# Optimization experiments

Measured on AMD Instinct MI355X. Metric: run time of the kernel, lower is better.

The kernel has to match this reference:

```python
import jax, jax.numpy as jnp
import numpy as np

D_MODEL = 1024
N_HEADS = 16
D_HEAD = 64
D_FF = 4096
WINDOW = 256
B, T = 2, 2048


def setup_inputs() -> dict:
    key = jax.random.key(0)
    ks = jax.random.split(key, 10)
    tot = N_HEADS * D_HEAD
    def w(k, shape):
        # approximate kaiming_normal_ fan_out init: std = sqrt(2/fan_out)
        fan_out = shape[0]
        return jax.random.normal(k, shape, jnp.float32) * np.sqrt(2.0 / fan_out)
    return {
        "x": jax.random.normal(ks[0], (B, T, D_MODEL), jnp.float32),
        "ln1_w": jnp.ones((D_MODEL,), jnp.float32),
        "qkv_w": w(ks[1], (3 * tot, D_MODEL)),
        "gate_w": w(ks[2], (tot, D_MODEL)),
        "out_w": w(ks[3], (D_MODEL, tot)),
        "ln2_w": jnp.ones((D_MODEL,), jnp.float32),
        "wg": w(ks[4], (D_FF, D_MODEL)),
        "wu": w(ks[5], (D_FF, D_MODEL)),
        "wo": w(ks[6], (D_MODEL, D_FF)),
    }


def _rmsnorm(x, w):
    return x * jax.lax.rsqrt(jnp.mean(x * x, axis=-1, keepdims=True) + 1e-6) * w


def _attention(x, qkv_w, gate_w, out_w):
    Bq, Tq, _ = x.shape
    tot = N_HEADS * D_HEAD
    qkv = x @ qkv_w.T  # [B,T,3*tot]
    q, k, v = jnp.split(qkv, 3, axis=-1)
    q = q.reshape(Bq, Tq, N_HEADS, D_HEAD).transpose(0, 2, 1, 3)
    k = k.reshape(Bq, Tq, N_HEADS, D_HEAD).transpose(0, 2, 1, 3)
    v = v.reshape(Bq, Tq, N_HEADS, D_HEAD).transpose(0, 2, 1, 3)
    scale = D_HEAD ** -0.5
    scores = jnp.einsum("bhqd,bhkd->bhqk", q, k) * scale
    pos = jnp.arange(Tq)
    dist = pos[:, None] - pos[None, :]
    allowed = (dist >= 0) & (dist < WINDOW)  # causal sliding window
    mask = jnp.where(allowed, 0.0, -jnp.inf).astype(scores.dtype)
    attn = jax.nn.softmax(scores + mask[None, None], axis=-1)
    out = jnp.einsum("bhqk,bhkd->bhqd", attn, v)
    out = out.transpose(0, 2, 1, 3).reshape(Bq, Tq, tot)
    gate = jax.nn.sigmoid(x @ gate_w.T)
    return (out * gate) @ out_w.T


def reference(x, ln1_w, qkv_w, gate_w, out_w, ln2_w, wg, wu, wo):
    x = x + _attention(_rmsnorm(x, ln1_w), qkv_w, gate_w, out_w)
    h = _rmsnorm(x, ln2_w)
    ffn = (jax.nn.silu(h @ wg.T) * (h @ wu.T)) @ wo.T
    return x + ffn
```

## Files before the change

kernel.cpp:

```cpp
#include <hip/hip_runtime.h>


#define DEV __device__ __forceinline__

using u16 = unsigned short;
typedef __attribute__((ext_vector_type(8))) short  short8;
typedef __attribute__((ext_vector_type(4))) float  floatx4;

DEV u16 f2bf(float f) {
  unsigned u = __builtin_bit_cast(unsigned, f);
  u += 0x7FFFu + ((u >> 16) & 1u);
  return (u16)(u >> 16);
}
DEV float bf2f(u16 h) {
  unsigned u = ((unsigned)h) << 16;
  return __builtin_bit_cast(float, u);
}
DEV floatx4 mfma16(short8 a, short8 b, floatx4 c) {
  return __builtin_amdgcn_mfma_f32_16x16x32_bf16(a, b, c, 0, 0, 0);
}
DEV void gload16(const u16* g, u16* lds_base_wave_uniform) {
  __builtin_amdgcn_global_load_lds(
      (const __attribute__((address_space(1))) void*)g,
      (__attribute__((address_space(3))) void*)lds_base_wave_uniform,
      16, 0, 0);
}

__global__ __launch_bounds__(256) void cvt_k(const float* __restrict__ in,
                                             u16* __restrict__ o) {
  const size_t i = (size_t)blockIdx.x * 256 + threadIdx.x;
  const float4 v = ((const float4*)in)[i];
  ushort4 r;
  r.x = f2bf(v.x); r.y = f2bf(v.y); r.z = f2bf(v.z); r.w = f2bf(v.w);
  ((ushort4*)o)[i] = r;
}

__global__ __launch_bounds__(256) void rmsnorm_k(const float* __restrict__ x,
                                                 const float* __restrict__ wt,
                                                 u16* __restrict__ o) {
  __shared__ float red[4];
  const int row = blockIdx.x;
  const int tid = threadIdx.x;
  const float4 v = ((const float4*)(x + (size_t)row * 1024))[tid];
  float ss = v.x * v.x + v.y * v.y + v.z * v.z + v.w * v.w;
  ss += __shfl_xor(ss, 1, 64);
  ss += __shfl_xor(ss, 2, 64);
  ss += __shfl_xor(ss, 4, 64);
  ss += __shfl_xor(ss, 8, 64);
  ss += __shfl_xor(ss, 16, 64);
  ss += __shfl_xor(ss, 32, 64);
  if ((tid & 63) == 0) red[tid >> 6] = ss;
  __syncthreads();
  const float tot = red[0] + red[1] + red[2] + red[3];
  const float sc = rsqrtf(tot * (1.0f / 1024.0f) + 1e-6f);
  const float4 wv = ((const float4*)wt)[tid];
  ushort4 r;
  r.x = f2bf(v.x * sc * wv.x);
  r.y = f2bf(v.y * sc * wv.y);
  r.z = f2bf(v.z * sc * wv.z);
  r.w = f2bf(v.w * sc * wv.w);
  ((ushort4*)(o + (size_t)row * 1024))[tid] = r;
}

template <int EPI>
__global__ __launch_bounds__(256) void gemm_bf16_k(
    const u16* __restrict__ A, const u16* __restrict__ B, int N, int K,
    u16* __restrict__ cb, float* __restrict__ cf,
    const u16* __restrict__ aux, const float* __restrict__ resid) {
  __shared__ __align__(16) u16 As[2][4096];
  __shared__ __align__(16) u16 Bs[2][4096];

  const int tid = threadIdx.x;
  const int w = tid >> 6, lane = tid & 63;
  const int wm = w >> 1, wn = w & 1;
  const int g = lane >> 4, r16 = lane & 15;
  const int m0 = blockIdx.y * 128, n0 = blockIdx.x * 128;

  const int crow = lane >> 2;
  const int ccol = (lane & 3) * 8;

  floatx4 acc[4][4];
#pragma unroll
  for (int i = 0; i < 4; i++)
#pragma unroll
    for (int j = 0; j < 4; j++) acc[i][j] = (floatx4){0.f, 0.f, 0.f, 0.f};

  const int nk = K >> 5;

  auto stage = [&](int buf, int k0) {
#pragma unroll
    for (int p = 0; p < 2; p++) {
      const int c = p * 4 + w;
      gload16(A + (size_t)(m0 + c * 16 + crow) * K + k0 + ccol, &As[buf][c * 512]);
      gload16(B + (size_t)(n0 + c * 16 + crow) * K + k0 + ccol, &Bs[buf][c * 512]);
    }
  };

  stage(0, 0);
  __syncthreads();

  for (int kt = 0; kt < nk; ++kt) {
    const int buf = kt & 1;
    if (kt + 1 < nk) stage(buf ^ 1, (kt + 1) * 32);
    short8 af[4], bfr[4];
#pragma unroll
    for (int i = 0; i < 4; i++)
      af[i] = *(const short8*)&As[buf][(wm * 64 + i * 16 + r16) * 32 + g * 8];
#pragma unroll
    for (int j = 0; j < 4; j++)
      bfr[j] = *(const short8*)&Bs[buf][(wn * 64 + j * 16 + r16) * 32 + g * 8];
#pragma unroll
    for (int i = 0; i < 4; i++)
#pragma unroll
      for (int j = 0; j < 4; j++) acc[i][j] = mfma16(af[i], bfr[j], acc[i][j]);
    __syncthreads();
  }

#pragma unroll
  for (int i = 0; i < 4; i++) {
    const int row = m0 + wm * 64 + i * 16 + g * 4;
#pragma unroll
    for (int j = 0; j < 4; j++) {
      const int col = n0 + wn * 64 + j * 16 + r16;
#pragma unroll
      for (int rr = 0; rr < 4; rr++) {
        const float v = acc[i][j][rr];
        const size_t idx = (size_t)(row + rr) * N + col;
        if constexpr (EPI == 0)      cb[idx] = f2bf(v);
        else if constexpr (EPI == 1) cb[idx] = f2bf(1.0f / (1.0f + __expf(-v)));
        else if constexpr (EPI == 2) cb[idx] = f2bf(v / (1.0f + __expf(-v)));
        else if constexpr (EPI == 3) cb[idx] = f2bf(v * bf2f(aux[idx]));
        else                         cf[idx] = v + resid[idx];
      }
    }
  }
}

__global__ __launch_bounds__(256) void attn_win_kernel(
    const u16* __restrict__ qkv, const u16* __restrict__ gate,
    u16* __restrict__ out) {
  __shared__ __align__(16) u16 Kl[64][80];
  __shared__ __align__(16) u16 Vt[64][80];
  __shared__ __align__(16) u16 Pl[4][16][80];

  const int tid = threadIdx.x;
  const int w = tid >> 6, lane = tid & 63;
  const int g = lane >> 4, r16 = lane & 15;

  const int q0 = blockIdx.x * 64;
  const int h = blockIdx.y;
  const int b = blockIdx.z;
  const u16* qb_ = qkv + (size_t)b * 2048 * 3072;

  const int tq = q0 + w * 16 + r16;
  const u16* qptr = qb_ + (size_t)tq * 3072 + h * 64;
  const short8 aq0 = *(const short8*)(qptr + g * 8);
  const short8 aq1 = *(const short8*)(qptr + 32 + g * 8);

  floatx4 O[4] = {{0,0,0,0},{0,0,0,0},{0,0,0,0},{0,0,0,0}};
  float mrow[4] = {-1e30f, -1e30f, -1e30f, -1e30f};
  float lrow[4] = {0.f, 0.f, 0.f, 0.f};

  const int srow = tid >> 2;
  const int sq4 = tid & 3;
  const int qw = q0 + w * 16;

  for (int kt = q0 - 256; kt <= q0; kt += 64) {
    if (kt < 0) continue;
    {
      const u16* kb = qb_ + (size_t)(kt + srow) * 3072 + 1024 + h * 64 + sq4 * 16;
      const short8 kv0 = *(const short8*)kb;
      const short8 kv1 = *(const short8*)(kb + 8);
      *(short8*)&Kl[srow][sq4 * 16] = kv0;
      *(short8*)&Kl[srow][sq4 * 16 + 8] = kv1;
      const u16* vb = kb + 1024;
      const short8 vv0 = *(const short8*)vb;
      const short8 vv1 = *(const short8*)(vb + 8);
#pragma unroll
      for (int j = 0; j < 8; j++) Vt[sq4 * 16 + j][srow] = (u16)vv0[j];
#pragma unroll
      for (int j = 0; j < 8; j++) Vt[sq4 * 16 + 8 + j][srow] = (u16)vv1[j];
    }
    __syncthreads();

    const bool active = (qw + 15 >= kt) && (qw - kt < 319);
    if (active) {
      floatx4 S[4];
#pragma unroll
      for (int nf = 0; nf < 4; nf++) {
        const short8 bk0 = *(const short8*)&Kl[nf * 16 + r16][g * 8];
        const short8 bk1 = *(const short8*)&Kl[nf * 16 + r16][32 + g * 8];
        floatx4 a = {0.f, 0.f, 0.f, 0.f};
        a = mfma16(aq0, bk0, a);
        a = mfma16(aq1, bk1, a);
        S[nf] = a;
      }
      float pm[4][4];
      float nmax[4] = {-1e30f, -1e30f, -1e30f, -1e30f};
#pragma unroll
      for (int nf = 0; nf < 4; nf++) {
        const int key = kt + nf * 16 + r16;
#pragma unroll
        for (int rr = 0; rr < 4; rr++) {
          const int q = qw + g * 4 + rr;
          const int dist = q - key;
          const float s = (dist >= 0 && dist < 256) ? S[nf][rr] : -1e30f;
          pm[nf][rr] = s;
          nmax[rr] = fmaxf(nmax[rr], s);
        }
      }
#pragma unroll
      for (int rr = 0; rr < 4; rr++) {
        float v = nmax[rr];
        v = fmaxf(v, __shfl_xor(v, 1, 64));
        v = fmaxf(v, __shfl_xor(v, 2, 64));
        v = fmaxf(v, __shfl_xor(v, 4, 64));
        v = fmaxf(v, __shfl_xor(v, 8, 64));
        const float mnew = fmaxf(mrow[rr], v);
        const float alpha = __expf(0.125f * (mrow[rr] - mnew));
        mrow[rr] = mnew;
        lrow[rr] *= alpha;
#pragma unroll
        for (int n = 0; n < 4; n++) O[n][rr] *= alpha;
        float ls = 0.f;
#pragma unroll
        for (int nf = 0; nf < 4; nf++) {
          const float s = pm[nf][rr];
          const float pv = (s < -1e29f) ? 0.f : __expf(0.125f * (s - mnew));
          pm[nf][rr] = pv;
          ls += pv;
        }
        ls += __shfl_xor(ls, 1, 64);
        ls += __shfl_xor(ls, 2, 64);
        ls += __shfl_xor(ls, 4, 64);
        ls += __shfl_xor(ls, 8, 64);
        lrow[rr] += ls;
      }
#pragma unroll
      for (int nf = 0; nf < 4; nf++)
#pragma unroll
        for (int rr = 0; rr < 4; rr++)
          Pl[w][g * 4 + rr][nf * 16 + r16] = f2bf(pm[nf][rr]);
#pragma unroll
      for (int kf = 0; kf < 2; kf++) {
        const short8 pa = *(const short8*)&Pl[w][r16][kf * 32 + g * 8];
#pragma unroll
        for (int n = 0; n < 4; n++) {
          const short8 vb8 = *(const short8*)&Vt[n * 16 + r16][kf * 32 + g * 8];
          O[n] = mfma16(pa, vb8, O[n]);
        }
      }
    }
    __syncthreads();
  }

#pragma unroll
  for (int n = 0; n < 4; n++) {
#pragma unroll
    for (int rr = 0; rr < 4; rr++) {
      const int t = qw + g * 4 + rr;
      const size_t idx = ((size_t)(b * 2048 + t)) * 1024 + h * 64 + n * 16 + r16;
      const float gv = bf2f(gate[idx]);
      const float ov = (O[n][rr] / lrow[rr]) * gv;
      out[idx] = f2bf(ov);
    }
  }
}

extern "C" void kernel_launch(void* const* d_in, const int* in_sizes, int n_in,
                              void* d_out, int out_size, void* d_ws,
                              size_t ws_size, hipStream_t stream) {
  (void)in_sizes; (void)n_in; (void)out_size; (void)ws_size;
  const float* x     = (const float*)d_in[0];
  const float* ln1   = (const float*)d_in[1];
  const float* qkvw  = (const float*)d_in[2];
  const float* gatew = (const float*)d_in[3];
  const float* outw  = (const float*)d_in[4];
  const float* ln2   = (const float*)d_in[5];
  const float* wg    = (const float*)d_in[6];
  const float* wu    = (const float*)d_in[7];
  const float* wo    = (const float*)d_in[8];
  float* outp = (float*)d_out;

  u16* p = (u16*)d_ws;
  u16* qkvw_b  = p; p += 3 * 1024 * 1024;
  u16* gatew_b = p; p += 1024 * 1024;
  u16* outw_b  = p; p += 1024 * 1024;
  u16* wg_b    = p; p += 4 * 1024 * 1024;
  u16* wu_b    = p; p += 4 * 1024 * 1024;
  u16* wo_b    = p; p += 4 * 1024 * 1024;
  u16* xn      = p; p += 4096 * 1024;
  u16* qkvb    = p; p += (size_t)4096 * 3072;
  u16* gates   = p; p += 4096 * 1024;
  u16* a3      = p; p += 4096 * 1024;
  u16* hb      = p; p += 4096 * 1024;
  u16* gs      = p; p += (size_t)4096 * 4096;
  float* x2    = (float*)p;

  cvt_k<<<3072, 256, 0, stream>>>(qkvw, qkvw_b);
  cvt_k<<<1024, 256, 0, stream>>>(gatew, gatew_b);
  cvt_k<<<1024, 256, 0, stream>>>(outw, outw_b);
  cvt_k<<<4096, 256, 0, stream>>>(wg, wg_b);
  cvt_k<<<4096, 256, 0, stream>>>(wu, wu_b);
  cvt_k<<<4096, 256, 0, stream>>>(wo, wo_b);

  rmsnorm_k<<<4096, 256, 0, stream>>>(x, ln1, xn);

  gemm_bf16_k<0><<<dim3(24, 32), 256, 0, stream>>>(xn, qkvw_b, 3072, 1024,
                                                   qkvb, nullptr, nullptr, nullptr);
  gemm_bf16_k<1><<<dim3(8, 32), 256, 0, stream>>>(xn, gatew_b, 1024, 1024,
                                                  gates, nullptr, nullptr, nullptr);

  attn_win_kernel<<<dim3(32, 16, 2), 256, 0, stream>>>(qkvb, gates, a3);

  gemm_bf16_k<4><<<dim3(8, 32), 256, 0, stream>>>(a3, outw_b, 1024, 1024,
                                                  nullptr, x2, nullptr, x);

  rmsnorm_k<<<4096, 256, 0, stream>>>(x2, ln2, hb);

  gemm_bf16_k<2><<<dim3(32, 32), 256, 0, stream>>>(hb, wg_b, 4096, 1024,
                                                   gs, nullptr, nullptr, nullptr);
  gemm_bf16_k<3><<<dim3(32, 32), 256, 0, stream>>>(hb, wu_b, 4096, 1024,
                                                   gs, nullptr, gs, nullptr);

  gemm_bf16_k<4><<<dim3(8, 32), 256, 0, stream>>>(gs, wo_b, 1024, 4096,
                                                  nullptr, outp, nullptr, x2);
}
```

Before: 445.2 us.

## Fuse weight casts, merge QKV+gate GEMM, split-K output GEMMs, swizzle blocks

```diff
diff --git a/kernel.cpp b/kernel.cpp
--- a/kernel.cpp
+++ b/kernel.cpp
@@ -26,13 +26,25 @@
       16, 0, 0);
 }
 
-__global__ __launch_bounds__(256) void cvt_k(const float* __restrict__ in,
-                                             u16* __restrict__ o) {
-  const size_t i = (size_t)blockIdx.x * 256 + threadIdx.x;
+__global__ __launch_bounds__(256) void cvt_all_k(
+    const float* __restrict__ s0, const float* __restrict__ s1,
+    const float* __restrict__ s2, const float* __restrict__ s3,
+    const float* __restrict__ s4, const float* __restrict__ s5,
+    u16* __restrict__ d0, u16* __restrict__ d1, u16* __restrict__ d2,
+    u16* __restrict__ d3, u16* __restrict__ d4, u16* __restrict__ d5) {
+  const int b = blockIdx.x;
+  const float* in; u16* out; int base;
+  if (b < 3072)       { in = s0; out = d0; base = 0; }
+  else if (b < 4096)  { in = s1; out = d1; base = 3072; }
+  else if (b < 5120)  { in = s2; out = d2; base = 4096; }
+  else if (b < 9216)  { in = s3; out = d3; base = 5120; }
+  else if (b < 13312) { in = s4; out = d4; base = 9216; }
+  else                { in = s5; out = d5; base = 13312; }
+  const size_t i = (size_t)(b - base) * 256 + threadIdx.x;
   const float4 v = ((const float4*)in)[i];
   ushort4 r;
   r.x = f2bf(v.x); r.y = f2bf(v.y); r.z = f2bf(v.z); r.w = f2bf(v.w);
-  ((ushort4*)o)[i] = r;
+  ((ushort4*)out)[i] = r;
 }
 
 __global__ __launch_bounds__(256) void rmsnorm_k(const float* __restrict__ x,
@@ -65,8 +77,8 @@
 template <int EPI>
 __global__ __launch_bounds__(256) void gemm_bf16_k(
     const u16* __restrict__ A, const u16* __restrict__ B, int N, int K,
-    u16* __restrict__ cb, float* __restrict__ cf,
-    const u16* __restrict__ aux, const float* __restrict__ resid) {
+    int ksz, u16* __restrict__ cb, float* __restrict__ cf,
+    const u16* __restrict__ aux, u16* __restrict__ cb2) {
   __shared__ __align__(16) u16 As[2][4096];
   __shared__ __align__(16) u16 Bs[2][4096];
 
@@ -74,7 +86,14 @@
   const int w = tid >> 6, lane = tid & 63;
   const int wm = w >> 1, wn = w & 1;
   const int g = lane >> 4, r16 = lane & 15;
-  const int m0 = blockIdx.y * 128, n0 = blockIdx.x * 128;
+
+  int bid = blockIdx.y * gridDim.x + blockIdx.x;
+  const int cpx = (gridDim.x * gridDim.y) >> 3;
+  bid = (bid & 7) * cpx + (bid >> 3);
+  const int m0 = (bid / gridDim.x) * 128;
+  const int n0 = (bid % gridDim.x) * 128;
+
+  const int kbeg = blockIdx.z * ksz;
 
   const int crow = lane >> 2;
   const int ccol = (lane & 3) * 8;
@@ -85,7 +104,7 @@
 #pragma unroll
     for (int j = 0; j < 4; j++) acc[i][j] = (floatx4){0.f, 0.f, 0.f, 0.f};
 
-  const int nk = K >> 5;
+  const int nk = ksz >> 5;
 
   auto stage = [&](int buf, int k0) {
 #pragma unroll
@@ -96,12 +115,12 @@
     }
   };
 
-  stage(0, 0);
+  stage(0, kbeg);
   __syncthreads();
 
   for (int kt = 0; kt < nk; ++kt) {
     const int buf = kt & 1;
-    if (kt + 1 < nk) stage(buf ^ 1, (kt + 1) * 32);
+    if (kt + 1 < nk) stage(buf ^ 1, kbeg + (kt + 1) * 32);
     short8 af[4], bfr[4];
 #pragma unroll
     for (int i = 0; i < 4; i++)
@@ -125,12 +144,20 @@
 #pragma unroll
       for (int rr = 0; rr < 4; rr++) {
         const float v = acc[i][j][rr];
-        const size_t idx = (size_t)(row + rr) * N + col;
-        if constexpr (EPI == 0)      cb[idx] = f2bf(v);
-        else if constexpr (EPI == 1) cb[idx] = f2bf(1.0f / (1.0f + __expf(-v)));
-        else if constexpr (EPI == 2) cb[idx] = f2bf(v / (1.0f + __expf(-v)));
-        else if constexpr (EPI == 3) cb[idx] = f2bf(v * bf2f(aux[idx]));
-        else                         cf[idx] = v + resid[idx];
+        if constexpr (EPI == 2) {
+          cb[(size_t)(row + rr) * N + col] = f2bf(v / (1.0f + __expf(-v)));
+        } else if constexpr (EPI == 3) {
+          const size_t idx = (size_t)(row + rr) * N + col;
+          cb[idx] = f2bf(v * bf2f(aux[idx]));
+        } else if constexpr (EPI == 5) {
+          atomicAdd(&cf[(size_t)(row + rr) * N + col], v);
+        } else if constexpr (EPI == 6) {
+          if (col < 3072)
+            cb[(size_t)(row + rr) * 3072 + col] = f2bf(v);
+          else
+            cb2[(size_t)(row + rr) * 1024 + (col - 3072)] =
+                f2bf(1.0f / (1.0f + __expf(-v)));
+        }
       }
     }
   }
@@ -297,32 +324,28 @@
   u16* gs      = p; p += (size_t)4096 * 4096;
   float* x2    = (float*)p;
 
-  cvt_k<<<3072, 256, 0, stream>>>(qkvw, qkvw_b);
-  cvt_k<<<1024, 256, 0, stream>>>(gatew, gatew_b);
-  cvt_k<<<1024, 256, 0, stream>>>(outw, outw_b);
-  cvt_k<<<4096, 256, 0, stream>>>(wg, wg_b);
-  cvt_k<<<4096, 256, 0, stream>>>(wu, wu_b);
-  cvt_k<<<4096, 256, 0, stream>>>(wo, wo_b);
+  cvt_all_k<<<17408, 256, 0, stream>>>(qkvw, gatew, outw, wg, wu, wo,
+                                       qkvw_b, gatew_b, outw_b, wg_b, wu_b, wo_b);
 
   rmsnorm_k<<<4096, 256, 0, stream>>>(x, ln1, xn);
 
-  gemm_bf16_k<0><<<dim3(24, 32), 256, 0, stream>>>(xn, qkvw_b, 3072, 1024,
-                                                   qkvb, nullptr, nullptr, nullptr);
-  gemm_bf16_k<1><<<dim3(8, 32), 256, 0, stream>>>(xn, gatew_b, 1024, 1024,
-                                                  gates, nullptr, nullptr, nullptr);
+  gemm_bf16_k<6><<<dim3(32, 32, 1), 256, 0, stream>>>(
+      xn, qkvw_b, 4096, 1024, 1024, qkvb, nullptr, nullptr, gates);
 
   attn_win_kernel<<<dim3(32, 16, 2), 256, 0, stream>>>(qkvb, gates, a3);
 
-  gemm_bf16_k<4><<<dim3(8, 32), 256, 0, stream>>>(a3, outw_b, 1024, 1024,
-                                                  nullptr, x2, nullptr, x);
+  hipMemcpyAsync(x2, x, (size_t)4096 * 1024 * 4, hipMemcpyDeviceToDevice, stream);
+  gemm_bf16_k<5><<<dim3(8, 32, 2), 256, 0, stream>>>(
+      a3, outw_b, 1024, 1024, 512, nullptr, x2, nullptr, nullptr);
 
   rmsnorm_k<<<4096, 256, 0, stream>>>(x2, ln2, hb);
 
-  gemm_bf16_k<2><<<dim3(32, 32), 256, 0, stream>>>(hb, wg_b, 4096, 1024,
-                                                   gs, nullptr, nullptr, nullptr);
-  gemm_bf16_k<3><<<dim3(32, 32), 256, 0, stream>>>(hb, wu_b, 4096, 1024,
-                                                   gs, nullptr, gs, nullptr);
-
-  gemm_bf16_k<4><<<dim3(8, 32), 256, 0, stream>>>(gs, wo_b, 1024, 4096,
-                                                  nullptr, outp, nullptr, x2);
-}
+  gemm_bf16_k<2><<<dim3(32, 32, 1), 256, 0, stream>>>(
+      hb, wg_b, 4096, 1024, 1024, gs, nullptr, nullptr, nullptr);
+  gemm_bf16_k<3><<<dim3(32, 32, 1), 256, 0, stream>>>(
+      hb, wu_b, 4096, 1024, 1024, gs, nullptr, gs, nullptr);
+
+  hipMemcpyAsync(outp, x2, (size_t)4096 * 1024 * 4, hipMemcpyDeviceToDevice, stream);
+  gemm_bf16_k<5><<<dim3(8, 32, 4), 256, 0, stream>>>(
+      gs, wo_b, 1024, 4096, 1024, nullptr, outp, nullptr, nullptr);
+}
```

Result: slower. 462.4 us (+3.9%).
